# Optimization experiments

Hardware: AMD Instinct MI355X
Metric: run time of the kernel (lower is better)

The kernel has to match this reference:

```python
import jax, jax.numpy as jnp
import numpy as np

N_IN, N_OUT, K, G = 128, 128, 3, 8
BATCH = 512
GRID_MIN, GRID_MAX = -1.0, 1.0
EDGES = N_IN * N_OUT


def setup_inputs() -> dict:
    key = jax.random.key(0)
    k1, k2 = jax.random.split(key)
    # inputs inside the grid range so splines are active
    x = jax.random.uniform(k1, (BATCH, N_IN), dtype=jnp.float32,
                           minval=GRID_MIN, maxval=GRID_MAX)
    # per-edge extended uniform knot vector: G+2K+1 points (k extra on each side)
    h = (GRID_MAX - GRID_MIN) / G
    knots_1d = jnp.linspace(GRID_MIN - K * h, GRID_MAX + K * h,
                            G + 2 * K + 1, dtype=jnp.float32)
    knots = jnp.broadcast_to(knots_1d, (EDGES, G + 2 * K + 1))
    c_basis = (jax.random.normal(k2, (EDGES, G + K), dtype=jnp.float32) * 0.1)
    c_spl = jnp.ones((N_OUT, N_IN), jnp.float32)
    c_res = jnp.ones((N_OUT, N_IN), jnp.float32)
    bias = jnp.zeros((N_OUT,), jnp.float32)
    return {"x": x, "knots": knots, "c_basis": c_basis,
            "c_spl": c_spl, "c_res": c_res, "bias": bias}


def _extend(x):
    # (batch, n_in) -> (edges, batch) with edge index = o*n_in + i
    batch = x.shape[0]
    return jnp.broadcast_to(x[:, None, :], (batch, N_OUT, N_IN)).reshape(batch, EDGES).T


def _basis(x, knots):
    # Cox-de Boor recursion; returns (edges, G+K, batch)
    x_ext = _extend(x)                   # (edges, batch)
    grid = knots[:, :, None]             # (edges, G+2K+1, 1)
    x_in = x_ext[:, None, :]             # (edges, 1, batch)
    b = ((x_in >= grid[:, :-1]) & (x_in < grid[:, 1:])).astype(jnp.float32)
    for order in range(1, K + 1):
        left = (x_in - grid[:, :-(order + 1)]) / (grid[:, order:-1] - grid[:, :-(order + 1)])
        right = (grid[:, order + 1:] - x_in) / (grid[:, order + 1:] - grid[:, 1:-order])
        b = left * b[:, :-1] + right * b[:, 1:]
    return b


def reference(x, knots, c_basis, c_spl, c_res, bias):
    batch = x.shape[0]
    bi = _basis(x, knots)                           # (edges, G+K, batch)
    spl = jnp.einsum('eg,egb->eb', c_basis, bi).T   # (batch, edges)
    y = c_spl.reshape(1, EDGES) * spl
    x_ext = _extend(x).T                            # (batch, edges)
    y = y + c_res.reshape(1, EDGES) * jax.nn.silu(x_ext)
    y = jnp.sum(y.reshape(batch, N_OUT, N_IN), axis=2) + bias
    return y
```

## Files before the change

### kernel.cpp

```cpp
#include <hip/hip_runtime.h>
#include <math.h>

#define N_IN  128
#define N_OUT 128
#define BATCH 512
#define NK    11
#define TBV   16
#define TOV   16
#define KTOT  1536

typedef float f32x4  __attribute__((ext_vector_type(4)));
typedef short bf16x8 __attribute__((ext_vector_type(8)));
typedef unsigned long long u64;

__device__ __forceinline__ unsigned short f2bf(float f) {
    unsigned u = __float_as_uint(f);
    u += 0x7FFFu + ((u >> 16) & 1u);
    return (unsigned short)(u >> 16);
}

__global__ __launch_bounds__(256) void pack_kernel(
    const float* __restrict__ x,      const float* __restrict__ cbasis,
    const float* __restrict__ cspl,   const float* __restrict__ cres,
    unsigned short* __restrict__ w2,  unsigned short* __restrict__ a2)
{
    if (blockIdx.x < 64) {
        const int e = blockIdx.x * 256 + threadIdx.x;
        const float s = cspl[e];
        const float* src = cbasis + (size_t)e * NK;
        unsigned short h[12];
        #pragma unroll
        for (int g = 0; g < NK; ++g) h[g] = f2bf(s * src[g]);
        h[11] = f2bf(cres[e]);
        unsigned d[6];
        #pragma unroll
        for (int j = 0; j < 6; ++j)
            d[j] = (unsigned)h[2 * j] | ((unsigned)h[2 * j + 1] << 16);
        unsigned short* dst = w2 + (size_t)e * 12;
        *(uint2*)(dst)     = make_uint2(d[0], d[1]);
        *(uint2*)(dst + 4) = make_uint2(d[2], d[3]);
        *(uint2*)(dst + 8) = make_uint2(d[4], d[5]);
    } else {
        const int p = (blockIdx.x - 64) * 256 + threadIdx.x;
        const float v = x[p];
        const float u = (v + 1.75f) * 4.0f;
        float jf = floorf(u);
        jf = fminf(fmaxf(jf, 3.0f), 10.0f);
        const float tt = u - jf;
        const float omt = 1.0f - tt;
        const float t2 = tt * tt, t3 = t2 * tt;
        const float B0 = omt * omt * omt * (1.0f / 6.0f);
        const float B1 = (3.0f * t3 - 6.0f * t2 + 4.0f) * (1.0f / 6.0f);
        const float B2 = (-3.0f * t3 + 3.0f * t2 + 3.0f * tt + 1.0f) * (1.0f / 6.0f);
        const float B3 = t3 * (1.0f / 6.0f);
        const int base = (int)jf - 3;
        const float sig = 1.0f / (1.0f + __expf(-v));
        const u64 v4 = (u64)f2bf(B0) | ((u64)f2bf(B1) << 16)
                     | ((u64)f2bf(B2) << 32) | ((u64)f2bf(B3) << 48);
        const int sh = base * 16;
        u64 q0, q1, q2;
        if (sh < 64) {
            q0 = v4 << sh;
            q1 = sh ? (v4 >> (64 - sh)) : 0ull;
            q2 = 0ull;
        } else {
            q0 = 0ull;
            q1 = v4 << (sh - 64);
            q2 = (sh > 64) ? (v4 >> (128 - sh)) : 0ull;
        }
        q2 |= (u64)f2bf(v * sig) << 48;
        u64* dst = (u64*)(a2 + (size_t)p * 12);
        dst[0] = q0; dst[1] = q1; dst[2] = q2;
    }
}

__global__ __launch_bounds__(512) void kan_kernel(
    const unsigned short* __restrict__ a2,
    const unsigned short* __restrict__ w2,
    const float* __restrict__ bias,
    float* __restrict__ y)
{
    __shared__ float sAcc[8 * 256];

    const int b0 = blockIdx.x * TBV;
    const int o0 = blockIdx.y * TOV;
    const int t  = threadIdx.x;
    const int w  = t >> 6;
    const int l  = t & 63;
    const int mn = l & 15;
    const int kq = (l >> 4) * 8;

    const unsigned short* ab = a2 + (size_t)(b0 + mn) * KTOT + w * 192 + kq;
    const unsigned short* wb = w2 + (size_t)(o0 + mn) * KTOT + w * 192 + kq;
    bf16x8 af[6], wf[6];
    #pragma unroll
    for (int s = 0; s < 6; ++s) {
        af[s] = *(const bf16x8*)(ab + s * 32);
        wf[s] = *(const bf16x8*)(wb + s * 32);
    }

    f32x4 acc = {0.f, 0.f, 0.f, 0.f};
    #pragma unroll
    for (int s = 0; s < 6; ++s)
        acc = __builtin_amdgcn_mfma_f32_16x16x32_bf16(af[s], wf[s], acc, 0, 0, 0);

    #pragma unroll
    for (int r = 0; r < 4; ++r)
        sAcc[w * 256 + ((l >> 4) * 4 + r) * 16 + mn] = acc[r];
    __syncthreads();
    if (t < 256) {
        const int m2 = t >> 4, n2 = t & 15;
        float sum = bias[o0 + n2];
        #pragma unroll
        for (int ww = 0; ww < 8; ++ww) sum += sAcc[ww * 256 + t];
        y[(b0 + m2) * N_OUT + (o0 + n2)] = sum;
    }
}

extern "C" void kernel_launch(void* const* d_in, const int* in_sizes, int n_in,
                              void* d_out, int out_size, void* d_ws, size_t ws_size,
                              hipStream_t stream) {
    const float* x      = (const float*)d_in[0];
    const float* cbasis = (const float*)d_in[2];
    const float* cspl   = (const float*)d_in[3];
    const float* cres   = (const float*)d_in[4];
    const float* bias   = (const float*)d_in[5];
    float* y = (float*)d_out;
    unsigned short* w2 = (unsigned short*)d_ws;
    unsigned short* a2 = (unsigned short*)((char*)d_ws + 512 * 1024);

    pack_kernel<<<320, 256, 0, stream>>>(x, cbasis, cspl, cres, w2, a2);
    dim3 grid(BATCH / TBV, N_OUT / TOV);
    kan_kernel<<<grid, 512, 0, stream>>>(a2, w2, bias, y);
}
```

Baseline: 68.01 us.

## Fuse pack and GEMM kernels into one cooperative launch with grid sync

Merges the packing kernel and the MFMA GEMM kernel into a single cooperative kernel of 256 blocks that packs weights and activations, does a grid-wide sync, then computes its output tile. The goal is to remove the second kernel launch and the gap between the two kernels. The grid sync adds its own barrier cost, and if the cooperative launch fails the code falls back to the original two-kernel path.

```diff
diff --git a/kernel.cpp b/kernel.cpp
--- a/kernel.cpp
+++ b/kernel.cpp
@@ -1,4 +1,5 @@
 #include <hip/hip_runtime.h>
+#include <hip/hip_cooperative_groups.h>
 #include <math.h>
 
 #define N_IN  128
@@ -8,6 +9,8 @@
 #define TBV   16
 #define TOV   16
 #define KTOT  1536
+
+namespace cg = cooperative_groups;
 
 typedef float f32x4  __attribute__((ext_vector_type(4)));
 typedef short bf16x8 __attribute__((ext_vector_type(8)));
@@ -19,72 +22,65 @@
     return (unsigned short)(u >> 16);
 }
 
-__global__ __launch_bounds__(256) void pack_kernel(
-    const float* __restrict__ x,      const float* __restrict__ cbasis,
-    const float* __restrict__ cspl,   const float* __restrict__ cres,
-    unsigned short* __restrict__ w2,  unsigned short* __restrict__ a2)
+__device__ __forceinline__ void pack_w_one(
+    int e, const float* __restrict__ cbasis, const float* __restrict__ cspl,
+    const float* __restrict__ cres, unsigned short* __restrict__ w2)
 {
-    if (blockIdx.x < 64) {
-        const int e = blockIdx.x * 256 + threadIdx.x;
-        const float s = cspl[e];
-        const float* src = cbasis + (size_t)e * NK;
-        unsigned short h[12];
-        #pragma unroll
-        for (int g = 0; g < NK; ++g) h[g] = f2bf(s * src[g]);
-        h[11] = f2bf(cres[e]);
-        unsigned d[6];
-        #pragma unroll
-        for (int j = 0; j < 6; ++j)
-            d[j] = (unsigned)h[2 * j] | ((unsigned)h[2 * j + 1] << 16);
-        unsigned short* dst = w2 + (size_t)e * 12;
-        *(uint2*)(dst)     = make_uint2(d[0], d[1]);
-        *(uint2*)(dst + 4) = make_uint2(d[2], d[3]);
-        *(uint2*)(dst + 8) = make_uint2(d[4], d[5]);
-    } else {
-        const int p = (blockIdx.x - 64) * 256 + threadIdx.x;
-        const float v = x[p];
-        const float u = (v + 1.75f) * 4.0f;
-        float jf = floorf(u);
-        jf = fminf(fmaxf(jf, 3.0f), 10.0f);
-        const float tt = u - jf;
-        const float omt = 1.0f - tt;
-        const float t2 = tt * tt, t3 = t2 * tt;
-        const float B0 = omt * omt * omt * (1.0f / 6.0f);
-        const float B1 = (3.0f * t3 - 6.0f * t2 + 4.0f) * (1.0f / 6.0f);
-        const float B2 = (-3.0f * t3 + 3.0f * t2 + 3.0f * tt + 1.0f) * (1.0f / 6.0f);
-        const float B3 = t3 * (1.0f / 6.0f);
-        const int base = (int)jf - 3;
-        const float sig = 1.0f / (1.0f + __expf(-v));
-        const u64 v4 = (u64)f2bf(B0) | ((u64)f2bf(B1) << 16)
-                     | ((u64)f2bf(B2) << 32) | ((u64)f2bf(B3) << 48);
-        const int sh = base * 16;
-        u64 q0, q1, q2;
-        if (sh < 64) {
-            q0 = v4 << sh;
-            q1 = sh ? (v4 >> (64 - sh)) : 0ull;
-            q2 = 0ull;
-        } else {
-            q0 = 0ull;
-            q1 = v4 << (sh - 64);
-            q2 = (sh > 64) ? (v4 >> (128 - sh)) : 0ull;
-        }
-        q2 |= (u64)f2bf(v * sig) << 48;
-        u64* dst = (u64*)(a2 + (size_t)p * 12);
-        dst[0] = q0; dst[1] = q1; dst[2] = q2;
-    }
+    const float s = cspl[e];
+    const float* src = cbasis + (size_t)e * NK;
+    unsigned short h[12];
+    #pragma unroll
+    for (int g = 0; g < NK; ++g) h[g] = f2bf(s * src[g]);
+    h[11] = f2bf(cres[e]);
+    unsigned d[6];
+    #pragma unroll
+    for (int j = 0; j < 6; ++j)
+        d[j] = (unsigned)h[2 * j] | ((unsigned)h[2 * j + 1] << 16);
+    unsigned short* dst = w2 + (size_t)e * 12;
+    *(uint2*)(dst)     = make_uint2(d[0], d[1]);
+    *(uint2*)(dst + 4) = make_uint2(d[2], d[3]);
+    *(uint2*)(dst + 8) = make_uint2(d[4], d[5]);
 }
 
-__global__ __launch_bounds__(512) void kan_kernel(
-    const unsigned short* __restrict__ a2,
-    const unsigned short* __restrict__ w2,
-    const float* __restrict__ bias,
-    float* __restrict__ y)
+__device__ __forceinline__ void pack_a_one(
+    int p, const float* __restrict__ x, unsigned short* __restrict__ a2)
 {
-    __shared__ float sAcc[8 * 256];
+    const float v = x[p];
+    const float u = (v + 1.75f) * 4.0f;
+    float jf = floorf(u);
+    jf = fminf(fmaxf(jf, 3.0f), 10.0f);
+    const float tt = u - jf;
+    const float omt = 1.0f - tt;
+    const float t2 = tt * tt, t3 = t2 * tt;
+    const float B0 = omt * omt * omt * (1.0f / 6.0f);
+    const float B1 = (3.0f * t3 - 6.0f * t2 + 4.0f) * (1.0f / 6.0f);
+    const float B2 = (-3.0f * t3 + 3.0f * t2 + 3.0f * tt + 1.0f) * (1.0f / 6.0f);
+    const float B3 = t3 * (1.0f / 6.0f);
+    const int base = (int)jf - 3;
+    const float sig = 1.0f / (1.0f + __expf(-v));
+    const u64 v4 = (u64)f2bf(B0) | ((u64)f2bf(B1) << 16)
+                 | ((u64)f2bf(B2) << 32) | ((u64)f2bf(B3) << 48);
+    const int sh = base * 16;
+    u64 q0, q1, q2;
+    if (sh < 64) {
+        q0 = v4 << sh;
+        q1 = sh ? (v4 >> (64 - sh)) : 0ull;
+        q2 = 0ull;
+    } else {
+        q0 = 0ull;
+        q1 = v4 << (sh - 64);
+        q2 = (sh > 64) ? (v4 >> (128 - sh)) : 0ull;
+    }
+    q2 |= (u64)f2bf(v * sig) << 48;
+    u64* dst = (u64*)(a2 + (size_t)p * 12);
+    dst[0] = q0; dst[1] = q1; dst[2] = q2;
+}
 
-    const int b0 = blockIdx.x * TBV;
-    const int o0 = blockIdx.y * TOV;
-    const int t  = threadIdx.x;
+__device__ __forceinline__ void gemm_tile(
+    int b0, int o0, int t,
+    const unsigned short* __restrict__ a2, const unsigned short* __restrict__ w2,
+    const float* __restrict__ bias, float* __restrict__ y, float* sAcc)
+{
     const int w  = t >> 6;
     const int l  = t & 63;
     const int mn = l & 15;
@@ -98,7 +94,6 @@
         af[s] = *(const bf16x8*)(ab + s * 32);
         wf[s] = *(const bf16x8*)(wb + s * 32);
     }
-
     f32x4 acc = {0.f, 0.f, 0.f, 0.f};
     #pragma unroll
     for (int s = 0; s < 6; ++s)
@@ -117,6 +112,50 @@
     }
 }
 
+__global__ __launch_bounds__(512) void kan_fused(
+    const float* __restrict__ x,      const float* __restrict__ cbasis,
+    const float* __restrict__ cspl,   const float* __restrict__ cres,
+    const float* __restrict__ bias,   unsigned short* __restrict__ w2,
+    unsigned short* __restrict__ a2,  float* __restrict__ y)
+{
+    __shared__ float sAcc[8 * 256];
+    const int t   = threadIdx.x;
+    const int gid = blockIdx.x * 512 + t;
+
+    if (gid < 16384) {
+        pack_w_one(gid, cbasis, cspl, cres, w2);
+    } else if (gid < 16384 + 65536) {
+        pack_a_one(gid - 16384, x, a2);
+    }
+
+    cg::this_grid().sync();
+
+    const int b0 = (blockIdx.x & 31) * TBV;
+    const int o0 = (blockIdx.x >> 5) * TOV;
+    gemm_tile(b0, o0, t, a2, w2, bias, y, sAcc);
+}
+
+__global__ __launch_bounds__(256) void pack_kernel(
+    const float* __restrict__ x,      const float* __restrict__ cbasis,
+    const float* __restrict__ cspl,   const float* __restrict__ cres,
+    unsigned short* __restrict__ w2,  unsigned short* __restrict__ a2)
+{
+    if (blockIdx.x < 64) {
+        pack_w_one(blockIdx.x * 256 + threadIdx.x, cbasis, cspl, cres, w2);
+    } else {
+        pack_a_one((blockIdx.x - 64) * 256 + threadIdx.x, x, a2);
+    }
+}
+
+__global__ __launch_bounds__(512) void kan_kernel(
+    const unsigned short* __restrict__ a2, const unsigned short* __restrict__ w2,
+    const float* __restrict__ bias, float* __restrict__ y)
+{
+    __shared__ float sAcc[8 * 256];
+    gemm_tile(blockIdx.x * TBV, blockIdx.y * TOV, threadIdx.x,
+              a2, w2, bias, y, sAcc);
+}
+
 extern "C" void kernel_launch(void* const* d_in, const int* in_sizes, int n_in,
                               void* d_out, int out_size, void* d_ws, size_t ws_size,
                               hipStream_t stream) {
@@ -129,7 +168,14 @@
     unsigned short* w2 = (unsigned short*)d_ws;
     unsigned short* a2 = (unsigned short*)((char*)d_ws + 512 * 1024);
 
-    pack_kernel<<<320, 256, 0, stream>>>(x, cbasis, cspl, cres, w2, a2);
-    dim3 grid(BATCH / TBV, N_OUT / TOV);
-    kan_kernel<<<grid, 512, 0, stream>>>(a2, w2, bias, y);
+    void* args[] = { (void*)&x, (void*)&cbasis, (void*)&cspl, (void*)&cres,
+                     (void*)&bias, (void*)&w2, (void*)&a2, (void*)&y };
+    hipError_t err = hipLaunchCooperativeKernel((const void*)kan_fused,
+                                                dim3(256), dim3(512),
+                                                args, 0, stream);
+    if (err != hipSuccess) {
+        pack_kernel<<<320, 256, 0, stream>>>(x, cbasis, cspl, cres, w2, a2);
+        dim3 grid(BATCH / TBV, N_OUT / TOV);
+        kan_kernel<<<grid, 512, 0, stream>>>(a2, w2, bias, y);
+    }
 }
```

Measured after the change: 116.1 us. 1.71x slower.
